# Performance work log

Hardware: AMD Instinct MI355X
Metric: run time of the kernel (lower is better)

Reference implementation:

```python
import jax, jax.numpy as jnp
import numpy as np

# Dimensions derived from LaneATTHead defaults (see shape_source)
B, CIN, CF, FH, FW = 8, 256, 64, 22, 40
A, S = 2784, 72          # n_anchors, n_offsets
NC = 2                   # num_category
D = CF * FH              # per-anchor feature dim = 1408
P = NC + 2 + 2 * S       # proposal dim = 148


def setup_inputs() -> dict:
    key = jax.random.key(0)
    ks = jax.random.split(key, 12)
    sc = 0.02
    return {
        "x": jax.random.normal(ks[0], (B, CIN, FH, FW), jnp.float32),
        "conv_w": jax.random.normal(ks[1], (CF, CIN), jnp.float32) * sc,
        "conv_b": jax.random.normal(ks[2], (CF,), jnp.float32) * sc,
        "attn_w": jax.random.normal(ks[3], (D, A - 1), jnp.float32) * sc,
        "attn_b": jax.random.normal(ks[4], (A - 1,), jnp.float32) * sc,
        "cls_w": jax.random.normal(ks[5], (2 * D, NC), jnp.float32) * sc,
        "cls_b": jax.random.normal(ks[6], (NC,), jnp.float32) * sc,
        "reg_w": jax.random.normal(ks[7], (2 * D, 2 * S), jnp.float32) * sc,
        "reg_b": jax.random.normal(ks[8], (2 * S,), jnp.float32) * sc,
        "anchors": jax.random.uniform(ks[9], (A, P), jnp.float32),
        "cut_xs": jax.random.randint(ks[10], (A, FH), 0, FW, jnp.int32),
        "invalid_mask": jax.random.randint(ks[11], (A, FH), 0, 2, jnp.int32).astype(jnp.bool_),
    }


def reference(x, conv_w, conv_b, attn_w, attn_b, cls_w, cls_b, reg_w, reg_b,
              anchors, cut_xs, invalid_mask):
    # 1x1 conv: [B,CIN,FH,FW] -> [B,CF,FH,FW]
    feats = jnp.einsum('bchw,oc->bohw', x, conv_w) + conv_b[None, :, None, None]

    # cut_anchor_features: gather per-anchor column per row, zero invalid
    rows = jnp.arange(FH)
    g = feats[:, :, rows[None, :], cut_xs]             # [B, CF, A, FH]
    g = jnp.transpose(g, (0, 2, 1, 3))                  # [B, A, CF, FH]
    g = jnp.where(invalid_mask[None, :, None, :], jnp.float32(0), g)
    baf = g.reshape(B, A, D)                            # [B, A, D]

    # attention over other anchors (softmax over A-1 slots)
    scores = baf @ attn_w + attn_b                      # [B, A, A-1]
    attention = jax.nn.softmax(scores, axis=-1)

    # scatter into [A,A] with zero diagonal (row-major off-diag fill, as in eye()+nonzero())
    i = jnp.arange(A)[:, None]
    k = jnp.arange(A - 1)[None, :]
    cols = k + (k >= i).astype(jnp.int32)               # [A, A-1]
    attn_mat = jnp.zeros((B, A, A), baf.dtype).at[:, i, cols].set(attention)

    # weighted pooling (equiv. of the transposed bmm chain)
    att_feat = jnp.einsum('bij,bjd->bid', attn_mat, baf)  # [B, A, D]

    f2 = jnp.concatenate([att_feat, baf], axis=-1)      # [B, A, 2D]
    cls = f2 @ cls_w + cls_b                            # [B, A, NC]
    reg = f2 @ reg_w + reg_b                            # [B, A, 2S]
    reg = jnp.concatenate([reg[..., :S], jax.nn.sigmoid(reg[..., S:])], axis=-1)

    base = jnp.broadcast_to(anchors, (B, A, P))
    # reg_proposals: [:, :, :NC]=cls ; [:, :, NC:NC+2]=anchor ; [:, :, NC+2:]+=reg
    props = jnp.concatenate([cls, base[..., NC:NC + 2], base[..., NC + 2:] + reg], axis=-1)
    return props, attn_mat
```

## Files before the change

kernel.cpp:

```cpp
#include <hip/hip_runtime.h>
#include <stdint.h>

typedef __attribute__((ext_vector_type(8))) __bf16 bf16x8;
typedef __attribute__((ext_vector_type(4))) float f32x4;
typedef __attribute__((ext_vector_type(2))) long long2v;
typedef unsigned short u16;
typedef unsigned char u8;

#define DEV static __device__ __forceinline__

constexpr int NB = 8;
constexpr int AA = 2784;
constexpr int AM1 = 2783;
constexpr int DD = 1408;
constexpr int MT = NB * AA;
constexpr int KP = 2816;

DEV u16 f2bf(float f) {
  uint32_t u = __builtin_bit_cast(uint32_t, f);
  u += 0x7FFFu + ((u >> 16) & 1u);
  return (u16)(u >> 16);
}
DEV float bf2f(unsigned v) { return __builtin_bit_cast(float, v << 16); }
DEV u8 f2f8(float f) {
  return (u8)(__builtin_amdgcn_cvt_pk_fp8_f32(f, f, 0, false) & 0xff);
}
DEV float4 cv4(unsigned w) {
  float4 r;
  r.x = __builtin_amdgcn_cvt_f32_fp8((int)w, 0);
  r.y = __builtin_amdgcn_cvt_f32_fp8((int)w, 1);
  r.z = __builtin_amdgcn_cvt_f32_fp8((int)w, 2);
  r.w = __builtin_amdgcn_cvt_f32_fp8((int)w, 3);
  return r;
}
DEV unsigned pk4(float a, float b, float c, float d) {
  int r = __builtin_amdgcn_cvt_pk_fp8_f32(a, b, 0, false);
  r = __builtin_amdgcn_cvt_pk_fp8_f32(c, d, r, true);
  return (unsigned)r;
}

DEV void load16_lds(const void* g, void* l) {
  auto gp = (const __attribute__((address_space(1))) uint32_t*)(uintptr_t)g;
  auto lp = (__attribute__((address_space(3))) uint32_t*)(uint32_t)(uintptr_t)l;
  __builtin_amdgcn_global_load_lds(gp, lp, 16, 0, 0);
}

#define VMW(n) asm volatile("s_waitcnt vmcnt(" #n ")" ::: "memory")
#define VMW0 asm volatile("s_waitcnt vmcnt(0)" ::: "memory")
#define LGW0 asm volatile("s_waitcnt lgkmcnt(0)" ::: "memory")
#define BARR asm volatile("s_barrier" ::: "memory")
#define SCHB __builtin_amdgcn_sched_barrier(0)

template <int QM>
DEV void mf32a(f32x4 (&acc)[8][4], const long (&Av)[4][2],
               const long (&bL)[2][2], const long (&bH)[2][2]) {
  __builtin_amdgcn_s_setprio(1);
#pragma unroll
  for (int mt = 0; mt < 4; ++mt)
#pragma unroll
    for (int nt = 0; nt < 2; ++nt)
#pragma unroll
      for (int ks = 0; ks < 2; ++ks)
        acc[QM * 4 + mt][nt] = __builtin_amdgcn_mfma_f32_16x16x32_fp8_fp8(
            Av[mt][ks], bL[nt][ks], acc[QM * 4 + mt][nt], 0, 0, 0);
#pragma unroll
  for (int mt = 0; mt < 4; ++mt)
#pragma unroll
    for (int nt = 0; nt < 2; ++nt)
#pragma unroll
      for (int ks = 0; ks < 2; ++ks)
        acc[QM * 4 + mt][2 + nt] = __builtin_amdgcn_mfma_f32_16x16x32_fp8_fp8(
            Av[mt][ks], bH[nt][ks], acc[QM * 4 + mt][2 + nt], 0, 0, 0);
  __builtin_amdgcn_s_setprio(0);
}
DEV void mf32b(f32x4 (&acc)[8][2], const long (&aL)[4][2],
               const long (&aH)[4][2], const long (&bb)[2][2]) {
  __builtin_amdgcn_s_setprio(1);
#pragma unroll
  for (int mt = 0; mt < 4; ++mt)
#pragma unroll
    for (int nt = 0; nt < 2; ++nt)
#pragma unroll
      for (int ks = 0; ks < 2; ++ks)
        acc[mt][nt] = __builtin_amdgcn_mfma_f32_16x16x32_fp8_fp8(
            aL[mt][ks], bb[nt][ks], acc[mt][nt], 0, 0, 0);
#pragma unroll
  for (int mt = 0; mt < 4; ++mt)
#pragma unroll
    for (int nt = 0; nt < 2; ++nt)
#pragma unroll
      for (int ks = 0; ks < 2; ++ks)
        acc[4 + mt][nt] = __builtin_amdgcn_mfma_f32_16x16x32_fp8_fp8(
            aH[mt][ks], bb[nt][ks], acc[4 + mt][nt], 0, 0, 0);
  __builtin_amdgcn_s_setprio(0);
}

__global__ __launch_bounds__(512) void gemm1_k(const u8* __restrict__ A,
                                               const u8* __restrict__ Bt,
                                               u8* __restrict__ outh,
                                               const float* __restrict__ b1) {
  constexpr int NT = 11;
  __shared__ __align__(16) u8 As8[2][32768];
  __shared__ __align__(16) u8 Bs8[2][32768];
  const int tid = threadIdx.x;
  const int lane = tid & 63;
  const int w = tid >> 6;
  const int wr = w >> 2, wc = w & 3;
  const int l16 = lane & 15, lq = lane >> 4;
  const int l7 = l16 & 7;

  const int gx = gridDim.x, gy = gridDim.y;
  const int nwg = gx * gy;
  const int i = blockIdx.x + blockIdx.y * gx;
  const int xcd = i & 7, pos = i >> 3;
  const int q = nwg >> 3, r = nwg & 7;
  const int lid = (xcd < r ? xcd * (q + 1) : r * (q + 1) + (xcd - r) * q) + pos;
  const int m0 = (lid / gy) * 256, n0 = (lid % gy) * 256;

  auto stA = [&](int buf, int half, int kt) {
#pragma unroll
    for (int inst = 0; inst < 2; ++inst) {
      int c = tid + inst * 512;
      int row = c >> 3, sl = c & 7;
      int sr = m0 + half * 128 + row;
      sr = sr < MT - 1 ? sr : MT - 1;
      load16_lds(A + (size_t)sr * 1408 + kt * 128 + ((sl ^ (row & 7)) << 4),
                 &As8[buf][half * 16384 + (c << 4)]);
    }
  };
  auto stB = [&](int buf, int half, int kt) {
#pragma unroll
    for (int inst = 0; inst < 2; ++inst) {
      int c = tid + inst * 512;
      int row = c >> 3, sl = c & 7;
      int sr = n0 + half * 128 + row;
      load16_lds(Bt + (size_t)sr * 1408 + kt * 128 + ((sl ^ (row & 7)) << 4),
                 &Bs8[buf][half * 16384 + (c << 4)]);
    }
  };
  auto rdA = [&](int buf, int qm, int kh, long (&a)[4][2]) {
    const int u = (kh * 4 + lq) ^ l7;
#pragma unroll
    for (int mt = 0; mt < 4; ++mt) {
      int rloc = qm * 64 + mt * 16 + l16;
      long2v v = *(const long2v*)&As8[buf][wr * 16384 + rloc * 128 + u * 16];
      a[mt][0] = v[0]; a[mt][1] = v[1];
    }
  };
  auto rdB = [&](int buf, int qn, int kh, long (&b)[2][2]) {
    const int u = (kh * 4 + lq) ^ l7;
#pragma unroll
    for (int nt = 0; nt < 2; ++nt) {
      int R = wc * 64 + qn * 32 + nt * 16 + l16;
      long2v v = *(const long2v*)&Bs8[buf][(R >> 7) * 16384 + (R & 127) * 128 + u * 16];
      b[nt][0] = v[0]; b[nt][1] = v[1];
    }
  };

  f32x4 acc[8][4];
#pragma unroll
  for (int i2 = 0; i2 < 8; ++i2)
#pragma unroll
    for (int j = 0; j < 4; ++j) acc[i2][j] = 0.f;

  long aL[4][2], aH[4][2], bL[2][2], bH[2][2];

  stA(0, 0, 0); stA(0, 1, 0); stB(0, 0, 0); stB(0, 1, 0);
  VMW0; BARR;
  int cur = 0;
  for (int t = 0; t < NT; ++t) {
    const bool tail = (t == NT - 1);
    const int nxt = cur ^ 1;
    rdA(cur, 0, 0, aL); rdB(cur, 0, 0, bL); rdB(cur, 1, 0, bH);
    if (!tail) { stA(nxt, 0, t + 1); stA(nxt, 1, t + 1); }
    BARR; LGW0; SCHB; mf32a<0>(acc, aL, bL, bH); BARR;
    rdA(cur, 1, 0, aH);
    if (!tail) { stB(nxt, 0, t + 1); stB(nxt, 1, t + 1); }
    BARR; LGW0; SCHB; mf32a<1>(acc, aH, bL, bH); BARR;
    rdA(cur, 0, 1, aL); rdB(cur, 0, 1, bL); rdB(cur, 1, 1, bH);
    BARR; LGW0; SCHB; mf32a<0>(acc, aL, bL, bH); BARR;
    rdA(cur, 1, 1, aH);
    if (!tail) VMW0;
    BARR; LGW0; SCHB; mf32a<1>(acc, aH, bL, bH); BARR;
    cur = nxt;
  }

#pragma unroll
  for (int mi = 0; mi < 8; ++mi)
#pragma unroll
    for (int r2 = 0; r2 < 4; ++r2) {
      int m = m0 + wr * 128 + mi * 16 + lq * 4 + r2;
      if (m >= MT) continue;
      int ii = m % AA;
#pragma unroll
      for (int ni = 0; ni < 4; ++ni) {
        int n = n0 + wc * 64 + ni * 16 + l16;
        if (n >= AM1) continue;
        int col = n + (n >= ii);
        outh[(size_t)m * KP + col] = f2f8(acc[mi][ni][r2] + b1[n]);
      }
    }
}

__global__ __launch_bounds__(512) void gemm2_k(const u8* __restrict__ A,
                                               const u8* __restrict__ Bt,
                                               u16* __restrict__ outh) {
  constexpr int NT = 22;
  __shared__ __align__(16) u8 As8[2][32768];
  __shared__ __align__(16) u8 Bs8[2][16384];
  const int tid = threadIdx.x;
  const int lane = tid & 63;
  const int w = tid >> 6;
  const int wr = w >> 2, wc = w & 3;
  const int l16 = lane & 15, lq = lane >> 4;
  const int l7 = l16 & 7;

  const int gx = gridDim.x, gy = gridDim.y;
  const int nwg = gx * gy;
  const int i = blockIdx.x + blockIdx.y * gx;
  const int xcd = i & 7, pos = i >> 3;
  const int q = nwg >> 3, r = nwg & 7;
  const int lid = (xcd < r ? xcd * (q + 1) : r * (q + 1) + (xcd - r) * q) + pos;
  const int m0 = (lid / gy) * 256, n0 = (lid % gy) * 128;

  const int bz = blockIdx.z;
  const u8* Ab = A + (size_t)bz * AA * KP;
  const u8* Bb = Bt + (size_t)bz * DD * KP;
  u16* outp = outh + (size_t)bz * AA * DD;

  auto stA = [&](int buf, int half, int kt) {
#pragma unroll
    for (int inst = 0; inst < 2; ++inst) {
      int c = tid + inst * 512;
      int row = c >> 3, sl = c & 7;
      int sr = m0 + half * 128 + row;
      sr = sr < AA - 1 ? sr : AA - 1;
      load16_lds(Ab + (size_t)sr * KP + kt * 128 + ((sl ^ (row & 7)) << 4),
                 &As8[buf][half * 16384 + (c << 4)]);
    }
  };
  auto stB = [&](int buf, int kt) {
#pragma unroll
    for (int inst = 0; inst < 2; ++inst) {
      int c = tid + inst * 512;
      int row = c >> 3, sl = c & 7;
      int sr = n0 + row;
      load16_lds(Bb + (size_t)sr * KP + kt * 128 + ((sl ^ (row & 7)) << 4),
                 &Bs8[buf][c << 4]);
    }
  };
  auto rdA = [&](int buf, int qm, int kh, long (&a)[4][2]) {
    const int u = (kh * 4 + lq) ^ l7;
#pragma unroll
    for (int mt = 0; mt < 4; ++mt) {
      int rloc = qm * 64 + mt * 16 + l16;
      long2v v = *(const long2v*)&As8[buf][wr * 16384 + rloc * 128 + u * 16];
      a[mt][0] = v[0]; a[mt][1] = v[1];
    }
  };
  auto rdB = [&](int buf, int kh, long (&b)[2][2]) {
    const int u = (kh * 4 + lq) ^ l7;
#pragma unroll
    for (int nt = 0; nt < 2; ++nt) {
      int R = wc * 32 + nt * 16 + l16;
      long2v v = *(const long2v*)&Bs8[buf][R * 128 + u * 16];
      b[nt][0] = v[0]; b[nt][1] = v[1];
    }
  };

  f32x4 acc[8][2];
#pragma unroll
  for (int i2 = 0; i2 < 8; ++i2)
#pragma unroll
    for (int j = 0; j < 2; ++j) acc[i2][j] = 0.f;

  long aL[4][2], aH[4][2], bb[2][2];

  stA(0, 0, 0); stA(0, 1, 0); stB(0, 0);
  VMW0; BARR;
  int cur = 0;
  for (int t = 0; t < NT; ++t) {
    const bool tail = (t == NT - 1);
    const int nxt = cur ^ 1;
    rdA(cur, 0, 0, aL); rdA(cur, 1, 0, aH); rdB(cur, 0, bb);
    if (!tail) { stA(nxt, 0, t + 1); stA(nxt, 1, t + 1); stB(nxt, t + 1); }
    BARR; LGW0; SCHB; mf32b(acc, aL, aH, bb); BARR;
    rdA(cur, 0, 1, aL); rdA(cur, 1, 1, aH); rdB(cur, 1, bb);
    if (!tail) VMW0;
    BARR; LGW0; SCHB; mf32b(acc, aL, aH, bb); BARR;
    cur = nxt;
  }

#pragma unroll
  for (int mi = 0; mi < 8; ++mi)
#pragma unroll
    for (int r2 = 0; r2 < 4; ++r2) {
      int m = m0 + wr * 128 + mi * 16 + lq * 4 + r2;
      if (m >= AA) continue;
      size_t base = (size_t)m * DD;
#pragma unroll
      for (int nt = 0; nt < 2; ++nt) {
        int n = n0 + wc * 32 + nt * 16 + l16;
        outp[base + n] = f2bf(acc[mi][nt][r2] * 0.00390625f);
      }
    }
}

__global__ __launch_bounds__(256) void conv_k(const float* __restrict__ x,
                                              const float* __restrict__ w,
                                              const float* __restrict__ bias,
                                              float* __restrict__ feats) {
  __shared__ float xs[256 * 40];
  int bb = blockIdx.x / 22, h = blockIdx.x % 22;
  const float* xp = x + (size_t)bb * 256 * 880 + h * 40;
  for (int l = threadIdx.x; l < 256 * 40; l += 256)
    xs[l] = xp[(l / 40) * 880 + (l % 40)];
  __syncthreads();
  for (int l = threadIdx.x; l < 64 * 40; l += 256) {
    int o = l / 40, ww = l % 40;
    float acc = bias[o];
    const float* wr = w + o * 256;
#pragma unroll 8
    for (int c = 0; c < 256; ++c) acc += xs[c * 40 + ww] * wr[c];
    feats[((size_t)(bb * 64 + o) * 22 + h) * 40 + ww] = acc;
  }
}

__global__ __launch_bounds__(256) void gt_k(const float* __restrict__ feats,
                                            const int* __restrict__ cut,
                                            const u8* __restrict__ inv,
                                            u16* __restrict__ baf,
                                            u8* __restrict__ baf8,
                                            u8* __restrict__ bft8) {
  unsigned probe = 0;
#pragma unroll
  for (int t = 0; t < 10; ++t)
    probe |= (unsigned)inv[4 * t + 1] | (unsigned)inv[4 * t + 2] | (unsigned)inv[4 * t + 3];
  const bool is_u8 = (probe != 0);
  __shared__ u8 t8[64][65];
  int a0 = blockIdx.x * 64, d0 = blockIdx.y * 64, b = blockIdx.z;
  int tx = threadIdx.x & 63, ty = threadIdx.x >> 6;
  int d = d0 + tx, o = d / 22, h = d - o * 22;
  for (int r = ty; r < 64; r += 4) {
    int a = a0 + r;
    u8 f8 = 0;
    if (a < AA) {
      int msk = is_u8 ? (int)inv[a * 22 + h] : ((const int*)inv)[a * 22 + h];
      float v = 0.f;
      if (!msk) v = feats[((size_t)(b * 64 + o) * 22 + h) * 40 + cut[a * 22 + h]];
      baf[((size_t)b * AA + a) * DD + d] = f2bf(v);
      f8 = f2f8(v);
      baf8[((size_t)b * AA + a) * DD + d] = f8;
    }
    t8[r][tx] = f8;
  }
  __syncthreads();
  for (int r = ty; r < 64; r += 4) {
    int a = a0 + tx;
    if (a < AA) bft8[((size_t)b * DD + d0 + r) * KP + a] = t8[tx][r];
  }
}

__global__ __launch_bounds__(256) void tr_attw_k(const float* __restrict__ w,
                                                 u8* __restrict__ wt8) {
  __shared__ u8 t8[64][65];
  int n0 = blockIdx.x * 64, k0 = blockIdx.y * 64;
  int tx = threadIdx.x & 63, ty = threadIdx.x >> 6;
  for (int r = ty; r < 64; r += 4) {
    int n = n0 + tx;
    t8[r][tx] = (n < AM1) ? f2f8(w[(size_t)(k0 + r) * AM1 + n]) : (u8)0;
  }
  __syncthreads();
  for (int r = ty; r < 64; r += 4)
    wt8[(size_t)(n0 + r) * 1408 + k0 + tx] = t8[tx][r];
}

__global__ __launch_bounds__(256) void wt_k(const float* __restrict__ cw,
                                            const float* __restrict__ rw,
                                            u16* __restrict__ wt) {
  int n = blockIdx.x;
  for (int k = threadIdx.x; k < 2816; k += 256) {
    float v = 0.f;
    if (n < 2) v = cw[(size_t)k * 2 + n];
    else if (n < 146) v = rw[(size_t)k * 144 + (n - 2)];
    wt[(size_t)n * 2816 + k] = f2bf(v);
  }
}

__global__ __launch_bounds__(256) void softf_k(u8* __restrict__ attP) {
  const int row = blockIdx.x;
  const int i = row % AA;
  u8* p = attP + (size_t)row * KP;
  const int t = threadIdx.x;
  const bool act = (t < 176);
  uint4 qw = act ? ((const uint4*)p)[t] : make_uint4(0, 0, 0, 0);
  float v[16];
  { float4 f = cv4(qw.x); v[0] = f.x; v[1] = f.y; v[2] = f.z; v[3] = f.w; }
  { float4 f = cv4(qw.y); v[4] = f.x; v[5] = f.y; v[6] = f.z; v[7] = f.w; }
  { float4 f = cv4(qw.z); v[8] = f.x; v[9] = f.y; v[10] = f.z; v[11] = f.w; }
  { float4 f = cv4(qw.w); v[12] = f.x; v[13] = f.y; v[14] = f.z; v[15] = f.w; }
  const int base = t * 16;
  float mx = -3e38f;
#pragma unroll
  for (int e = 0; e < 16; ++e) {
    int j = base + e;
    if (act && j < AA && j != i) mx = fmaxf(mx, v[e]);
  }
#pragma unroll
  for (int o = 1; o < 64; o <<= 1) mx = fmaxf(mx, __shfl_xor(mx, o));
  __shared__ float rm[4], rs[4];
  if (!(t & 63)) rm[t >> 6] = mx;
  __syncthreads();
  mx = fmaxf(fmaxf(rm[0], rm[1]), fmaxf(rm[2], rm[3]));
  float s = 0.f, ev[16];
#pragma unroll
  for (int e = 0; e < 16; ++e) {
    int j = base + e;
    float tv = (act && j < AA && j != i) ? __expf(v[e] - mx) : 0.f;
    ev[e] = tv; s += tv;
  }
#pragma unroll
  for (int o = 1; o < 64; o <<= 1) s += __shfl_xor(s, o);
  if (!(t & 63)) rs[t >> 6] = s;
  __syncthreads();
  s = (rs[0] + rs[1]) + (rs[2] + rs[3]);
  const float inv = 256.f / s;
#pragma unroll
  for (int e = 0; e < 16; ++e) ev[e] *= inv;
  if (act) {
    uint4 ow;
    ow.x = pk4(ev[0], ev[1], ev[2], ev[3]);
    ow.y = pk4(ev[4], ev[5], ev[6], ev[7]);
    ow.z = pk4(ev[8], ev[9], ev[10], ev[11]);
    ow.w = pk4(ev[12], ev[13], ev[14], ev[15]);
    ((uint4*)p)[t] = ow;
  }
}

__global__ __launch_bounds__(256) void exp_k(const u8* __restrict__ src,
                                             float* __restrict__ dst) {
  int row = blockIdx.x;
  int t = threadIdx.x;
  if (t >= 174) return;
  uint4 qw = ((const uint4*)(src + (size_t)row * KP))[t];
  const float is = 0.00390625f;
  float4 f0 = cv4(qw.x), f1 = cv4(qw.y), f2 = cv4(qw.z), f3 = cv4(qw.w);
  float4* dp = (float4*)(dst + (size_t)row * AA + t * 16);
  dp[0] = make_float4(f0.x * is, f0.y * is, f0.z * is, f0.w * is);
  dp[1] = make_float4(f1.x * is, f1.y * is, f1.z * is, f1.w * is);
  dp[2] = make_float4(f2.x * is, f2.y * is, f2.z * is, f2.w * is);
  dp[3] = make_float4(f3.x * is, f3.y * is, f3.z * is, f3.w * is);
}

__global__ __launch_bounds__(256) void head_k(const u16* __restrict__ A1,
                                              const u16* __restrict__ A2,
                                              const u16* __restrict__ Bt,
                                              float* __restrict__ outf,
                                              const float* __restrict__ b1,
                                              const float* __restrict__ b2,
                                              const float* __restrict__ anch) {
  constexpr int K = 2816, NT = K / 32, BN = 160, HN = 80, NF = 5;
  __shared__ __align__(16) u16 As[2][128 * 32];
  __shared__ __align__(16) u16 Bs[2][BN * 32 + 512];
  const int tid = threadIdx.x;
  const int lane = tid & 63;
  const int wm = tid >> 7, wn = (tid >> 6) & 1;
  const int m0 = blockIdx.x * 128;
  const int l16 = lane & 15, lq = lane >> 4;

  auto stage = [&](int buf, int t) {
    const int k0 = t * 32;
    const u16* Asrc = (k0 < 1408) ? A1 : A2;
    const int kk = (k0 < 1408) ? k0 : k0 - 1408;
#pragma unroll
    for (int inst = 0; inst < 2; ++inst) {
      int c = tid + inst * 256;
      load16_lds(Asrc + (size_t)(m0 + (c >> 2)) * 1408 + kk + (c & 3) * 8, &As[buf][c * 8]);
    }
#pragma unroll
    for (int inst = 0; inst < 3; ++inst) {
      int c = tid + inst * 256;
      int ce = c < BN * 4 ? c : BN * 4 - 1;
      load16_lds(Bt + (size_t)(ce >> 2) * K + k0 + (ce & 3) * 8, &Bs[buf][ce * 8]);
    }
  };

  f32x4 acc[4][NF];
#pragma unroll
  for (int i = 0; i < 4; ++i)
#pragma unroll
    for (int j = 0; j < NF; ++j) acc[i][j] = 0.f;

  stage(0, 0);
  stage(1, 1);
  for (int t = 0; t < NT; ++t) {
    if (t + 1 < NT) VMW(5); else VMW0;
    BARR;
    const int cur = t & 1;
    bf16x8 av[4], bv[NF];
#pragma unroll
    for (int mt = 0; mt < 4; ++mt)
      av[mt] = *(const bf16x8*)&As[cur][(wm * 64 + mt * 16 + l16) * 32 + lq * 8];
#pragma unroll
    for (int nt = 0; nt < NF; ++nt)
      bv[nt] = *(const bf16x8*)&Bs[cur][(wn * HN + nt * 16 + l16) * 32 + lq * 8];
#pragma unroll
    for (int mt = 0; mt < 4; ++mt)
#pragma unroll
      for (int nt = 0; nt < NF; ++nt)
        acc[mt][nt] = __builtin_amdgcn_mfma_f32_16x16x32_bf16(av[mt], bv[nt], acc[mt][nt], 0, 0, 0);
    BARR;
    if (t + 2 < NT) stage(cur, t + 2);
  }

#pragma unroll
  for (int nt = 0; nt < NF; ++nt) {
    int n = wn * HN + nt * 16 + l16;
    if (n >= 146) continue;
#pragma unroll
    for (int mt = 0; mt < 4; ++mt)
#pragma unroll
      for (int r = 0; r < 4; ++r) {
        int m = m0 + wm * 64 + mt * 16 + lq * 4 + r;
        int ii = m % AA;
        float v = acc[mt][nt][r];
        if (n < 2) {
          outf[(size_t)m * 148 + n] = v + b1[n];
          if (n == 0) {
            outf[(size_t)m * 148 + 2] = anch[ii * 148 + 2];
            outf[(size_t)m * 148 + 3] = anch[ii * 148 + 3];
          }
        } else {
          int rr = n - 2;
          v += b2[rr];
          if (rr >= 72) v = 1.f / (1.f + __expf(-v));
          outf[(size_t)m * 148 + 4 + rr] = anch[ii * 148 + 4 + rr] + v;
        }
      }
  }
}

extern "C" void kernel_launch(void* const* d_in, const int* in_sizes, int n_in,
                              void* d_out, int out_size, void* d_ws, size_t ws_size,
                              hipStream_t stream) {
  const float* x       = (const float*)d_in[0];
  const float* conv_w  = (const float*)d_in[1];
  const float* conv_b  = (const float*)d_in[2];
  const float* attn_w  = (const float*)d_in[3];
  const float* attn_b  = (const float*)d_in[4];
  const float* cls_w   = (const float*)d_in[5];
  const float* cls_b   = (const float*)d_in[6];
  const float* reg_w   = (const float*)d_in[7];
  const float* reg_b   = (const float*)d_in[8];
  const float* anchors = (const float*)d_in[9];
  const int*   cut_xs  = (const int*)d_in[10];
  const u8*    inv     = (const u8*)d_in[11];

  float* props = (float*)d_out;
  float* attn  = props + (size_t)MT * 148;
  u16* attf = (u16*)attn;

  char* wp = (char*)d_ws;
  auto take = [&](size_t bytes) { char* p = wp; wp += (bytes + 255) & ~(size_t)255; return p; };
  u16* baf    = (u16*)take((size_t)MT * DD * 2);
  u8*  baf8   = (u8*)take((size_t)MT * DD);
  u8*  baft8  = (u8*)take((size_t)NB * DD * KP);
  u8*  attP8  = (u8*)take((size_t)MT * KP);
  u8*  attwt8 = (u8*)take((size_t)KP * 1408);
  float* feats = (float*)take((size_t)450560 * 4);
  u16* wt      = (u16*)take((size_t)160 * 2816 * 2);

  conv_k<<<dim3(176), 256, 0, stream>>>(x, conv_w, conv_b, feats);
  gt_k<<<dim3(44, 22, 8), 256, 0, stream>>>(feats, cut_xs, inv, baf, baf8, baft8);
  tr_attw_k<<<dim3(44, 22), 256, 0, stream>>>(attn_w, attwt8);
  wt_k<<<dim3(160), 256, 0, stream>>>(cls_w, reg_w, wt);

  gemm1_k<<<dim3(87, 11), 512, 0, stream>>>(baf8, attwt8, attP8, attn_b);
  softf_k<<<dim3(MT), 256, 0, stream>>>(attP8);
  gemm2_k<<<dim3(11, 11, 8), 512, 0, stream>>>(attP8, baft8, attf);
  head_k<<<dim3(174), 256, 0, stream>>>(attf, baf, wt, props,
                                        cls_b, reg_b, anchors);
  exp_k<<<dim3(MT), 256, 0, stream>>>(attP8, attn);
}
```

Measured before the change: 710.2 us.

## Unify FP8 GEMMs into one templated kernel with triple-buffered LDS pipeline

Merges the two FP8 GEMM kernels into one templated kernel that uses a 256x128 tile and a three-stage LDS ring, prefetching two K-tiles ahead with partial vmcnt waits. The per-k-step barriers drop from four or two to one. gemm1 moves from 256x256 tiles on an 87x11 grid to 256x128 tiles on an 87x22 grid. The aim is to hide global-to-LDS latency and cut synchronisation, at the cost of 144KB LDS per block and reloading the A operand twice in gemm1.

```diff
diff --git a/kernel.cpp b/kernel.cpp
--- a/kernel.cpp
+++ b/kernel.cpp
@@ -51,163 +51,32 @@
 #define BARR asm volatile("s_barrier" ::: "memory")
 #define SCHB __builtin_amdgcn_sched_barrier(0)
 
-template <int QM>
-DEV void mf32a(f32x4 (&acc)[8][4], const long (&Av)[4][2],
-               const long (&bL)[2][2], const long (&bH)[2][2]) {
+DEV void mf32(f32x4 (&acc)[8][2], const long (&a)[8][2], const long (&b)[2][2]) {
   __builtin_amdgcn_s_setprio(1);
 #pragma unroll
-  for (int mt = 0; mt < 4; ++mt)
-#pragma unroll
-    for (int nt = 0; nt < 2; ++nt)
-#pragma unroll
-      for (int ks = 0; ks < 2; ++ks)
-        acc[QM * 4 + mt][nt] = __builtin_amdgcn_mfma_f32_16x16x32_fp8_fp8(
-            Av[mt][ks], bL[nt][ks], acc[QM * 4 + mt][nt], 0, 0, 0);
-#pragma unroll
-  for (int mt = 0; mt < 4; ++mt)
-#pragma unroll
-    for (int nt = 0; nt < 2; ++nt)
-#pragma unroll
-      for (int ks = 0; ks < 2; ++ks)
-        acc[QM * 4 + mt][2 + nt] = __builtin_amdgcn_mfma_f32_16x16x32_fp8_fp8(
-            Av[mt][ks], bH[nt][ks], acc[QM * 4 + mt][2 + nt], 0, 0, 0);
-  __builtin_amdgcn_s_setprio(0);
-}
-DEV void mf32b(f32x4 (&acc)[8][2], const long (&aL)[4][2],
-               const long (&aH)[4][2], const long (&bb)[2][2]) {
-  __builtin_amdgcn_s_setprio(1);
-#pragma unroll
-  for (int mt = 0; mt < 4; ++mt)
+  for (int mt = 0; mt < 8; ++mt)
 #pragma unroll
     for (int nt = 0; nt < 2; ++nt)
 #pragma unroll
       for (int ks = 0; ks < 2; ++ks)
         acc[mt][nt] = __builtin_amdgcn_mfma_f32_16x16x32_fp8_fp8(
-            aL[mt][ks], bb[nt][ks], acc[mt][nt], 0, 0, 0);
-#pragma unroll
-  for (int mt = 0; mt < 4; ++mt)
-#pragma unroll
-    for (int nt = 0; nt < 2; ++nt)
-#pragma unroll
-      for (int ks = 0; ks < 2; ++ks)
-        acc[4 + mt][nt] = __builtin_amdgcn_mfma_f32_16x16x32_fp8_fp8(
-            aH[mt][ks], bb[nt][ks], acc[4 + mt][nt], 0, 0, 0);
+            a[mt][ks], b[nt][ks], acc[mt][nt], 0, 0, 0);
   __builtin_amdgcn_s_setprio(0);
 }
 
-__global__ __launch_bounds__(512) void gemm1_k(const u8* __restrict__ A,
-                                               const u8* __restrict__ Bt,
-                                               u8* __restrict__ outh,
-                                               const float* __restrict__ b1) {
-  constexpr int NT = 11;
-  __shared__ __align__(16) u8 As8[2][32768];
-  __shared__ __align__(16) u8 Bs8[2][32768];
-  const int tid = threadIdx.x;
-  const int lane = tid & 63;
-  const int w = tid >> 6;
-  const int wr = w >> 2, wc = w & 3;
-  const int l16 = lane & 15, lq = lane >> 4;
-  const int l7 = l16 & 7;
-
-  const int gx = gridDim.x, gy = gridDim.y;
-  const int nwg = gx * gy;
-  const int i = blockIdx.x + blockIdx.y * gx;
-  const int xcd = i & 7, pos = i >> 3;
-  const int q = nwg >> 3, r = nwg & 7;
-  const int lid = (xcd < r ? xcd * (q + 1) : r * (q + 1) + (xcd - r) * q) + pos;
-  const int m0 = (lid / gy) * 256, n0 = (lid % gy) * 256;
-
-  auto stA = [&](int buf, int half, int kt) {
-#pragma unroll
-    for (int inst = 0; inst < 2; ++inst) {
-      int c = tid + inst * 512;
-      int row = c >> 3, sl = c & 7;
-      int sr = m0 + half * 128 + row;
-      sr = sr < MT - 1 ? sr : MT - 1;
-      load16_lds(A + (size_t)sr * 1408 + kt * 128 + ((sl ^ (row & 7)) << 4),
-                 &As8[buf][half * 16384 + (c << 4)]);
-    }
-  };
-  auto stB = [&](int buf, int half, int kt) {
-#pragma unroll
-    for (int inst = 0; inst < 2; ++inst) {
-      int c = tid + inst * 512;
-      int row = c >> 3, sl = c & 7;
-      int sr = n0 + half * 128 + row;
-      load16_lds(Bt + (size_t)sr * 1408 + kt * 128 + ((sl ^ (row & 7)) << 4),
-                 &Bs8[buf][half * 16384 + (c << 4)]);
-    }
-  };
-  auto rdA = [&](int buf, int qm, int kh, long (&a)[4][2]) {
-    const int u = (kh * 4 + lq) ^ l7;
-#pragma unroll
-    for (int mt = 0; mt < 4; ++mt) {
-      int rloc = qm * 64 + mt * 16 + l16;
-      long2v v = *(const long2v*)&As8[buf][wr * 16384 + rloc * 128 + u * 16];
-      a[mt][0] = v[0]; a[mt][1] = v[1];
-    }
-  };
-  auto rdB = [&](int buf, int qn, int kh, long (&b)[2][2]) {
-    const int u = (kh * 4 + lq) ^ l7;
-#pragma unroll
-    for (int nt = 0; nt < 2; ++nt) {
-      int R = wc * 64 + qn * 32 + nt * 16 + l16;
-      long2v v = *(const long2v*)&Bs8[buf][(R >> 7) * 16384 + (R & 127) * 128 + u * 16];
-      b[nt][0] = v[0]; b[nt][1] = v[1];
-    }
-  };
-
-  f32x4 acc[8][4];
-#pragma unroll
-  for (int i2 = 0; i2 < 8; ++i2)
-#pragma unroll
-    for (int j = 0; j < 4; ++j) acc[i2][j] = 0.f;
-
-  long aL[4][2], aH[4][2], bL[2][2], bH[2][2];
-
-  stA(0, 0, 0); stA(0, 1, 0); stB(0, 0, 0); stB(0, 1, 0);
-  VMW0; BARR;
-  int cur = 0;
-  for (int t = 0; t < NT; ++t) {
-    const bool tail = (t == NT - 1);
-    const int nxt = cur ^ 1;
-    rdA(cur, 0, 0, aL); rdB(cur, 0, 0, bL); rdB(cur, 1, 0, bH);
-    if (!tail) { stA(nxt, 0, t + 1); stA(nxt, 1, t + 1); }
-    BARR; LGW0; SCHB; mf32a<0>(acc, aL, bL, bH); BARR;
-    rdA(cur, 1, 0, aH);
-    if (!tail) { stB(nxt, 0, t + 1); stB(nxt, 1, t + 1); }
-    BARR; LGW0; SCHB; mf32a<1>(acc, aH, bL, bH); BARR;
-    rdA(cur, 0, 1, aL); rdB(cur, 0, 1, bL); rdB(cur, 1, 1, bH);
-    BARR; LGW0; SCHB; mf32a<0>(acc, aL, bL, bH); BARR;
-    rdA(cur, 1, 1, aH);
-    if (!tail) VMW0;
-    BARR; LGW0; SCHB; mf32a<1>(acc, aH, bL, bH); BARR;
-    cur = nxt;
-  }
-
-#pragma unroll
-  for (int mi = 0; mi < 8; ++mi)
-#pragma unroll
-    for (int r2 = 0; r2 < 4; ++r2) {
-      int m = m0 + wr * 128 + mi * 16 + lq * 4 + r2;
-      if (m >= MT) continue;
-      int ii = m % AA;
-#pragma unroll
-      for (int ni = 0; ni < 4; ++ni) {
-        int n = n0 + wc * 64 + ni * 16 + l16;
-        if (n >= AM1) continue;
-        int col = n + (n >= ii);
-        outh[(size_t)m * KP + col] = f2f8(acc[mi][ni][r2] + b1[n]);
-      }
-    }
-}
-
-__global__ __launch_bounds__(512) void gemm2_k(const u8* __restrict__ A,
-                                               const u8* __restrict__ Bt,
-                                               u16* __restrict__ outh) {
-  constexpr int NT = 22;
-  __shared__ __align__(16) u8 As8[2][32768];
-  __shared__ __align__(16) u8 Bs8[2][16384];
+template <int MODE>
+__global__ __launch_bounds__(512) void gemm_k(const u8* __restrict__ A,
+                                              const u8* __restrict__ Bt,
+                                              u8* __restrict__ out8,
+                                              u16* __restrict__ outh,
+                                              const float* __restrict__ b1) {
+  constexpr int K   = (MODE == 1) ? 1408 : KP;
+  constexpr int NT  = K / 128;
+  constexpr int LDA = (MODE == 1) ? 1408 : KP;
+  constexpr int LDB = (MODE == 1) ? 1408 : KP;
+  constexpr int MR  = (MODE == 1) ? MT : AA;
+  __shared__ __align__(16) u8 As8[3][32768];
+  __shared__ __align__(16) u8 Bs8[3][16384];
   const int tid = threadIdx.x;
   const int lane = tid & 63;
   const int w = tid >> 6;
@@ -223,20 +92,25 @@
   const int lid = (xcd < r ? xcd * (q + 1) : r * (q + 1) + (xcd - r) * q) + pos;
   const int m0 = (lid / gy) * 256, n0 = (lid % gy) * 128;
 
-  const int bz = blockIdx.z;
-  const u8* Ab = A + (size_t)bz * AA * KP;
-  const u8* Bb = Bt + (size_t)bz * DD * KP;
-  u16* outp = outh + (size_t)bz * AA * DD;
-
-  auto stA = [&](int buf, int half, int kt) {
-#pragma unroll
-    for (int inst = 0; inst < 2; ++inst) {
+  const u8* Ab = A;
+  const u8* Bb = Bt;
+  u16* outp = outh;
+  if constexpr (MODE == 2) {
+    const int bz = blockIdx.z;
+    Ab += (size_t)bz * AA * KP;
+    Bb += (size_t)bz * DD * KP;
+    outp += (size_t)bz * AA * DD;
+  }
+
+  auto stA = [&](int buf, int kt) {
+#pragma unroll
+    for (int inst = 0; inst < 4; ++inst) {
       int c = tid + inst * 512;
       int row = c >> 3, sl = c & 7;
-      int sr = m0 + half * 128 + row;
-      sr = sr < AA - 1 ? sr : AA - 1;
-      load16_lds(Ab + (size_t)sr * KP + kt * 128 + ((sl ^ (row & 7)) << 4),
-                 &As8[buf][half * 16384 + (c << 4)]);
+      int sr = m0 + row;
+      sr = sr < MR - 1 ? sr : MR - 1;
+      load16_lds(Ab + (size_t)sr * LDA + kt * 128 + ((sl ^ (row & 7)) << 4),
+                 &As8[buf][c << 4]);
     }
   };
   auto stB = [&](int buf, int kt) {
@@ -245,16 +119,16 @@
       int c = tid + inst * 512;
       int row = c >> 3, sl = c & 7;
       int sr = n0 + row;
-      load16_lds(Bb + (size_t)sr * KP + kt * 128 + ((sl ^ (row & 7)) << 4),
+      load16_lds(Bb + (size_t)sr * LDB + kt * 128 + ((sl ^ (row & 7)) << 4),
                  &Bs8[buf][c << 4]);
     }
   };
-  auto rdA = [&](int buf, int qm, int kh, long (&a)[4][2]) {
+  auto rdA = [&](int buf, int kh, long (&a)[8][2]) {
     const int u = (kh * 4 + lq) ^ l7;
 #pragma unroll
-    for (int mt = 0; mt < 4; ++mt) {
-      int rloc = qm * 64 + mt * 16 + l16;
-      long2v v = *(const long2v*)&As8[buf][wr * 16384 + rloc * 128 + u * 16];
+    for (int mt = 0; mt < 8; ++mt) {
+      int rloc = wr * 128 + mt * 16 + l16;
+      long2v v = *(const long2v*)&As8[buf][rloc * 128 + u * 16];
       a[mt][0] = v[0]; a[mt][1] = v[1];
     }
   };
@@ -274,36 +148,56 @@
 #pragma unroll
     for (int j = 0; j < 2; ++j) acc[i2][j] = 0.f;
 
-  long aL[4][2], aH[4][2], bb[2][2];
-
-  stA(0, 0, 0); stA(0, 1, 0); stB(0, 0);
-  VMW0; BARR;
-  int cur = 0;
+  long a[8][2], b[2][2];
+
+  stA(0, 0); stB(0, 0);
+  stA(1, 1); stB(1, 1);
+  VMW(6);
+  BARR;
+
   for (int t = 0; t < NT; ++t) {
-    const bool tail = (t == NT - 1);
-    const int nxt = cur ^ 1;
-    rdA(cur, 0, 0, aL); rdA(cur, 1, 0, aH); rdB(cur, 0, bb);
-    if (!tail) { stA(nxt, 0, t + 1); stA(nxt, 1, t + 1); stB(nxt, t + 1); }
-    BARR; LGW0; SCHB; mf32b(acc, aL, aH, bb); BARR;
-    rdA(cur, 0, 1, aL); rdA(cur, 1, 1, aH); rdB(cur, 1, bb);
-    if (!tail) VMW0;
-    BARR; LGW0; SCHB; mf32b(acc, aL, aH, bb); BARR;
-    cur = nxt;
-  }
-
-#pragma unroll
-  for (int mi = 0; mi < 8; ++mi)
-#pragma unroll
-    for (int r2 = 0; r2 < 4; ++r2) {
-      int m = m0 + wr * 128 + mi * 16 + lq * 4 + r2;
-      if (m >= AA) continue;
-      size_t base = (size_t)m * DD;
-#pragma unroll
-      for (int nt = 0; nt < 2; ++nt) {
-        int n = n0 + wc * 32 + nt * 16 + l16;
-        outp[base + n] = f2bf(acc[mi][nt][r2] * 0.00390625f);
+    const int c = t % 3, s = (t + 2) % 3;
+    if (t + 2 < NT) { stA(s, t + 2); stB(s, t + 2); }
+    rdA(c, 0, a); rdB(c, 0, b);
+    LGW0; SCHB;
+    mf32(acc, a, b);
+    rdA(c, 1, a); rdB(c, 1, b);
+    LGW0; SCHB;
+    mf32(acc, a, b);
+    if (t + 2 < NT) VMW(6); else if (t + 1 < NT) VMW0;
+    if (t + 1 < NT) BARR;
+  }
+
+  if constexpr (MODE == 1) {
+#pragma unroll
+    for (int mi = 0; mi < 8; ++mi)
+#pragma unroll
+      for (int r2 = 0; r2 < 4; ++r2) {
+        int m = m0 + wr * 128 + mi * 16 + lq * 4 + r2;
+        int ii = m % AA;
+#pragma unroll
+        for (int ni = 0; ni < 2; ++ni) {
+          int n = n0 + wc * 32 + ni * 16 + l16;
+          if (n >= AM1) continue;
+          int col = n + (n >= ii);
+          out8[(size_t)m * KP + col] = f2f8(acc[mi][ni][r2] + b1[n]);
+        }
       }
-    }
+  } else {
+#pragma unroll
+    for (int mi = 0; mi < 8; ++mi)
+#pragma unroll
+      for (int r2 = 0; r2 < 4; ++r2) {
+        int m = m0 + wr * 128 + mi * 16 + lq * 4 + r2;
+        if (m >= AA) continue;
+        size_t base = (size_t)m * DD;
+#pragma unroll
+        for (int ni = 0; ni < 2; ++ni) {
+          int n = n0 + wc * 32 + ni * 16 + l16;
+          outp[base + n] = f2bf(acc[mi][ni][r2] * 0.00390625f);
+        }
+      }
+  }
 }
 
 __global__ __launch_bounds__(256) void conv_k(const float* __restrict__ x,
@@ -575,9 +469,9 @@
   tr_attw_k<<<dim3(44, 22), 256, 0, stream>>>(attn_w, attwt8);
   wt_k<<<dim3(160), 256, 0, stream>>>(cls_w, reg_w, wt);
 
-  gemm1_k<<<dim3(87, 11), 512, 0, stream>>>(baf8, attwt8, attP8, attn_b);
+  gemm_k<1><<<dim3(87, 22), 512, 0, stream>>>(baf8, attwt8, attP8, nullptr, attn_b);
   softf_k<<<dim3(MT), 256, 0, stream>>>(attP8);
-  gemm2_k<<<dim3(11, 11, 8), 512, 0, stream>>>(attP8, baft8, attf);
+  gemm_k<2><<<dim3(11, 11, 8), 512, 0, stream>>>(attP8, baft8, nullptr, attf, nullptr);
   head_k<<<dim3(174), 256, 0, stream>>>(attf, baf, wt, props,
                                         cls_b, reg_b, anchors);
   exp_k<<<dim3(MT), 256, 0, stream>>>(attP8, attn);
```

After: 707.9 us. Within noise of the previous version (-0.3%).
